# Optimization experiments

Measured on AMD Instinct MI355X. Metric: run time of the kernel, lower is better.

## Reference

```python
import jax, jax.numpy as jnp
import numpy as np

B, S, N, D, O = 64, 512, 128, 768, 3


def _xavier(k, shape):
    lim = (6.0 / (shape[0] + shape[1])) ** 0.5
    return jax.random.uniform(k, shape, jnp.float32, -lim, lim)


def setup_inputs() -> dict:
    key = jax.random.key(0)
    ks = jax.random.split(key, 16)
    sentence_embed = jax.random.normal(ks[0], (B, S, D), jnp.float32)
    # sparse binary dependency-graph adjacencies
    dg = (jax.random.uniform(ks[1], (B, N, N)) < 0.08).astype(jnp.float32)
    dg1 = (jax.random.uniform(ks[2], (B, N, N)) < 0.08).astype(jnp.float32)
    # target token span inside the sentence: [start, end), end > start
    start = jax.random.randint(ks[3], (B,), 1, 400)
    length = jax.random.randint(ks[4], (B,), 1, 16)
    target_span = jnp.stack([start, start + length], -1).astype(jnp.int32)
    # contiguous subword spans per GCN node (tran_indices), non-overlapping
    lens = jax.random.randint(ks[5], (B, N), 1, 4)
    ends = jnp.minimum(jnp.cumsum(lens, axis=1), S - 2)
    starts = jnp.concatenate([jnp.zeros((B, 1), ends.dtype), ends[:, :-1]], axis=1)
    tran_spans = jnp.stack([starts, ends], -1).astype(jnp.int32)  # [B,N,2]
    # node span of the target in the GCN graph (span_indices[i][0])
    gs = jax.random.randint(ks[6], (B,), 0, N - 8)
    gl = jax.random.randint(ks[7], (B,), 1, 8)
    gcn_span = jnp.stack([gs, gs + gl], -1).astype(jnp.int32)
    # parameters
    W_proj = _xavier(ks[8], (D, D))
    Wg1 = _xavier(ks[9], (D, D))
    Wg2 = _xavier(ks[10], (D, D))
    Wg3 = _xavier(ks[11], (D, D))
    stdv = 1.0 / np.sqrt(D)
    bg1 = jax.random.uniform(ks[12], (D,), jnp.float32, -stdv, stdv)
    bg2 = jax.random.uniform(ks[13], (D,), jnp.float32, -stdv, stdv)
    bg3 = jax.random.uniform(ks[14], (D,), jnp.float32, -stdv, stdv)
    fc_W = _xavier(ks[15], (2 * D, O))
    fc_b = jnp.zeros((O,), jnp.float32)
    return dict(sentence_embed=sentence_embed, dg=dg, dg1=dg1, W_proj=W_proj,
                Wg1=Wg1, bg1=bg1, Wg2=Wg2, bg2=bg2, Wg3=Wg3, bg3=bg3,
                fc_W=fc_W, fc_b=fc_b, target_span=target_span,
                tran_spans=tran_spans, gcn_span=gcn_span)


def reference(sentence_embed, dg, dg1, W_proj, Wg1, bg1, Wg2, bg2, Wg3, bg3,
              fc_W, fc_b, target_span, tran_spans, gcn_span):
    dt = sentence_embed.dtype
    pos = jnp.arange(S)
    # --- ragged target max-pool over sentence_embed[l:r] -> [B, D] ---
    tmask = (pos[None, :] >= target_span[:, 0:1]) & (pos[None, :] < target_span[:, 1:2])
    neg = jnp.finfo(dt).min
    target_max = jnp.max(jnp.where(tmask[:, :, None], sentence_embed, neg), axis=1)
    # --- ragged span-sum into GCN node features (tran_indices loop) -> [B, N, D] ---
    # torch slices [s+1 : e+1]
    nmask = ((pos[None, None, :] >= tran_spans[..., 0:1] + 1) &
             (pos[None, None, :] < tran_spans[..., 1:2] + 1)).astype(dt)  # [B,N,S]
    tmps = jnp.einsum('bns,bsd->bnd', nmask, sentence_embed)
    # --- GCN stack (GraphConvolution, bigcn=False) ---
    x = jax.nn.relu(tmps @ W_proj)
    adj = dg + dg1
    adj = jnp.where(adj >= 1, jnp.ones((), dt), adj)
    denom = jnp.sum(adj, axis=2, keepdims=True) + 1e-07
    def gcn(h, W, b):
        return jnp.einsum('bnm,bmd->bnd', adj, h @ W) / denom + b
    x = jax.nn.relu(gcn(x, Wg1, bg1)) + x
    x = jax.nn.relu(gcn(x, Wg2, bg2)) + x
    x = jax.nn.relu(gcn(x, Wg3, bg3)) + x
    # --- ragged node-span sum over GCN output -> [B, D] ---
    npos = jnp.arange(N)
    gmask = ((npos[None, :] >= gcn_span[:, 0:1]) & (npos[None, :] < gcn_span[:, 1:2])).astype(dt)
    gcn_target = jnp.einsum('bn,bnd->bd', gmask, x)
    # --- head ---
    logits = jnp.tanh(jnp.concatenate([target_max, gcn_target], axis=1) @ fc_W + fc_b)
    return logits
```

## Files before the change

kernel.cpp:

```cpp
#include <hip/hip_runtime.h>
#include <float.h>
#include <math.h>

typedef __attribute__((ext_vector_type(8))) short short8;
typedef __attribute__((ext_vector_type(4))) float f32x4;
typedef __attribute__((ext_vector_type(4))) unsigned short u16x4;
typedef unsigned short u16;
typedef unsigned int u32;

constexpr int B_ = 64, S_ = 512, N_ = 128, D_ = 768;

__device__ inline u16 f2h(float x) {
    _Float16 hh = (_Float16)x;
    return __builtin_bit_cast(u16, hh);
}
__device__ inline float h2f(u16 h) {
    return (float)__builtin_bit_cast(_Float16, h);
}

__device__ inline void gload_lds16(const u16* g, u16* s) {
    __builtin_amdgcn_global_load_lds(
        (const __attribute__((address_space(1))) u32*)g,
        (__attribute__((address_space(3))) u32*)s, 16, 0, 0);
}

__device__ inline int fragIdx(int row, int col) {
    return ((row >> 4) * 24 + (col >> 5)) * 512 + ((col >> 3) & 3) * 128
         + (row & 15) * 8 + (col & 7);
}

__global__ __launch_bounds__(192)
void span_split_kernel(const float* __restrict__ se, const int* __restrict__ spans,
                       u16* __restrict__ th) {
    const int bn = blockIdx.x;
    const int b  = bn >> 7;
    const int s  = spans[bn * 2 + 0];
    const int e  = spans[bn * 2 + 1];
    const float* base = se + (size_t)b * S_ * D_;
    const int d4 = threadIdx.x;
    float4 acc = make_float4(0.f, 0.f, 0.f, 0.f);
    for (int r = s + 1; r <= e; ++r) {
        const float4 v = reinterpret_cast<const float4*>(base + (size_t)r * D_)[d4];
        acc.x += v.x; acc.y += v.y; acc.z += v.z; acc.w += v.w;
    }
    u16x4 hv;
    hv[0] = f2h(acc.x); hv[1] = f2h(acc.y);
    hv[2] = f2h(acc.z); hv[3] = f2h(acc.w);
    *(u16x4*)(th + fragIdx(bn, d4 * 4)) = hv;
}

__global__ __launch_bounds__(192)
void target_max_kernel(const float* __restrict__ se, const int* __restrict__ tspan,
                       float* __restrict__ tmax) {
    const int b = blockIdx.x;
    const int c = blockIdx.y * 192 + threadIdx.x;
    const int s = tspan[b * 2 + 0];
    const int e = tspan[b * 2 + 1];
    const float* base = se + (size_t)b * S_ * D_ + c;
    float m = -FLT_MAX;
    for (int r = s; r < e; ++r) m = fmaxf(m, base[(size_t)r * D_]);
    tmax[(size_t)b * D_ + c] = m;
}

__global__ __launch_bounds__(128)
void adj_kernel(const float* __restrict__ dg, const float* __restrict__ dg1,
                u16* __restrict__ adj, float* __restrict__ invden) {
    const int row = blockIdx.x;
    const int t   = threadIdx.x;
    const size_t idx = (size_t)row * N_ + t;
    float a = dg[idx] + dg1[idx];
    a = (a >= 1.f) ? 1.f : a;
    adj[idx] = f2h(a);
    float w = a;
    #pragma unroll
    for (int off = 32; off; off >>= 1) w += __shfl_down(w, off, 64);
    __shared__ float ssum[2];
    if ((t & 63) == 0) ssum[t >> 6] = w;
    __syncthreads();
    if (t == 0) invden[row] = 1.f / (ssum[0] + ssum[1] + 1e-7f);
}

__global__ __launch_bounds__(256)
void wsplit_kernel(const float* __restrict__ W0, const float* __restrict__ W1,
                   const float* __restrict__ W2, const float* __restrict__ W3,
                   u16* __restrict__ wth) {
    __shared__ float t[64][65];
    const int mi = blockIdx.z;
    const float* W = (mi == 0) ? W0 : (mi == 1) ? W1 : (mi == 2) ? W2 : W3;
    const int k0 = blockIdx.y * 64, n0 = blockIdx.x * 64;
    #pragma unroll 4
    for (int it = 0; it < 16; ++it) {
        const int lin = it * 256 + threadIdx.x;
        const int r = lin >> 6, c = lin & 63;
        t[r][c] = W[(size_t)(k0 + r) * D_ + n0 + c];
    }
    __syncthreads();
    u16* oh = wth + (size_t)mi * D_ * D_;
    #pragma unroll 4
    for (int it = 0; it < 16; ++it) {
        const int lin = it * 256 + threadIdx.x;
        const int r = lin >> 6, c = lin & 63;
        oh[(size_t)(n0 + r) * D_ + k0 + c] = f2h(t[c][r]);
    }
}

template<int MODE>
__global__ __launch_bounds__(512, 4)
void gemm_fused(const u16* __restrict__ Ah,
                const u16* __restrict__ Bh,
                const u16* __restrict__ ADJ, const float* __restrict__ invden,
                const float* __restrict__ bias,
                u16* __restrict__ Oh) {
    __shared__ u16 lds[21504];
    const int tid  = threadIdx.x;
    const int lane = tid & 63, w = tid >> 6;
    const int wr = w >> 1, wc = w & 1;
    const int lr = lane & 15, lh = lane >> 4;

    int bid = blockIdx.x;
    bid = (bid & 7) * 64 + (bid >> 3);
    const int bnb = bid & 7, bmb = bid >> 3;
    const int bn = bnb * 96;

    const int qch = (lane & 3) ^ ((lane >> 3) & 3);
    const u16* gBsrc = Bh + (size_t)(bn + w * 16 + (lane >> 2)) * 768 + qch * 8;

    const int mblk0 = bmb * 8 + wr * 2;
    const u16* gAstage = Ah + (size_t)(bmb * 8 + w) * 12288 + lane * 8;

    f32x4 acc[2][3];
    #pragma unroll
    for (int i = 0; i < 2; ++i)
        #pragma unroll
        for (int j = 0; j < 3; ++j)
            acc[i][j] = (f32x4){0.f, 0.f, 0.f, 0.f};

    gload_lds16(gAstage, lds + w * 512);
    if (w < 6) gload_lds16(gBsrc, lds + 12288 + w * 512);
    gload_lds16(gAstage + 512, lds + 4096 + w * 512);
    if (w < 6) gload_lds16(gBsrc + 32, lds + 12288 + 3072 + w * 512);

    const int pB = (lh ^ ((lr >> 1) & 3)) << 3;
    const int aOff0 = (wr * 2) * 512 + lane * 8;
    const int aOff1 = (wr * 2 + 1) * 512 + lane * 8;

#define GEMM_ITER(C)                                                          \
    {                                                                         \
        const int t_ = 3 * tt + (C);                                          \
        if (t_ <= 22) {                                                       \
            if (w < 6) asm volatile("s_waitcnt vmcnt(2)" ::: "memory");       \
            else       asm volatile("s_waitcnt vmcnt(1)" ::: "memory");       \
        } else {                                                              \
            asm volatile("s_waitcnt vmcnt(0)" ::: "memory");                  \
        }                                                                     \
        __builtin_amdgcn_s_barrier();                                         \
        __builtin_amdgcn_sched_barrier(0);                                    \
        if (t_ <= 21) {                                                       \
            gload_lds16(gAstage + (t_ + 2) * 512,                             \
                        lds + (((C) + 2) % 3) * 4096 + w * 512);              \
            if (w < 6)                                                        \
                gload_lds16(gBsrc + (t_ + 2) * 32,                            \
                            lds + 12288 + (((C) + 2) % 3) * 3072 + w * 512);  \
        }                                                                     \
        const u16* La = lds + ((C) % 3) * 4096;                               \
        const u16* Lb = lds + 12288 + ((C) % 3) * 3072;                       \
        short8 aF[2], bF[3];                                                  \
        aF[0] = *(const short8*)&La[aOff0];                                   \
        aF[1] = *(const short8*)&La[aOff1];                                   \
        _Pragma("unroll")                                                     \
        for (int f = 0; f < 3; ++f)                                           \
            bF[f] = *(const short8*)&Lb[(wc * 48 + f * 16 + lr) * 32 + pB];   \
        __builtin_amdgcn_s_setprio(1);                                        \
        _Pragma("unroll")                                                     \
        for (int mf = 0; mf < 2; ++mf)                                        \
            _Pragma("unroll")                                                 \
            for (int nf = 0; nf < 3; ++nf)                                    \
                acc[mf][nf] = __builtin_amdgcn_mfma_f32_16x16x32_f16(aF[mf], bF[nf], acc[mf][nf], 0, 0, 0); \
        __builtin_amdgcn_s_setprio(0);                                        \
    }

    for (int tt = 0; tt < 8; ++tt) {
        GEMM_ITER(0)
        GEMM_ITER(1)
        GEMM_ITER(2)
    }
#undef GEMM_ITER

    if (MODE == 0) {
        #pragma unroll
        for (int mf = 0; mf < 2; ++mf) {
            const int mblk = mblk0 + mf;
            #pragma unroll
            for (int r = 0; r < 4; ++r) {
                const int lane_r = lh * 4 + r;
                #pragma unroll
                for (int nf = 0; nf < 3; ++nf) {
                    const int c = bn + wc * 48 + nf * 16 + lr;
                    const int idx = (mblk * 24 + (c >> 5)) * 512
                                  + ((c >> 3) & 3) * 128 + lane_r * 8 + (c & 7);
                    Oh[idx] = f2h(fmaxf(acc[mf][nf][r], 0.f));
                }
            }
        }
        return;
    }

    __builtin_amdgcn_s_barrier();
    __builtin_amdgcn_sched_barrier(0);

    const u16* adjb = ADJ + (size_t)bmb * (N_ * N_);
    short8 adjr[8];
    #pragma unroll
    for (int mf = 0; mf < 2; ++mf)
        #pragma unroll
        for (int ks = 0; ks < 4; ++ks)
            adjr[mf * 4 + ks] = *(const short8*)(adjb +
                (size_t)(wr * 32 + mf * 16 + lr) * 128 + ks * 32 + lh * 8);

    u16* hwT = lds;
    #pragma unroll
    for (int mf = 0; mf < 2; ++mf) {
        const int node0 = wr * 32 + mf * 16 + lh * 4;
        #pragma unroll
        for (int nf = 0; nf < 3; ++nf) {
            const int c = wc * 48 + nf * 16 + lr;
            u16x4 hv;
            #pragma unroll
            for (int r = 0; r < 4; ++r) hv[r] = f2h(acc[mf][nf][r]);
            *(u16x4*)&hwT[c * 128 + (((node0 >> 3) ^ (c & 7)) << 3) + (node0 & 7)] = hv;
        }
    }
    asm volatile("s_waitcnt lgkmcnt(0)" ::: "memory");
    __builtin_amdgcn_s_barrier();
    __builtin_amdgcn_sched_barrier(0);

    f32x4 acc2[2][3];
    #pragma unroll
    for (int i = 0; i < 2; ++i)
        #pragma unroll
        for (int j = 0; j < 3; ++j)
            acc2[i][j] = (f32x4){0.f, 0.f, 0.f, 0.f};

    #pragma unroll
    for (int ks = 0; ks < 4; ++ks) {
        short8 bf[3];
        #pragma unroll
        for (int f = 0; f < 3; ++f) {
            const int c = wc * 48 + f * 16 + lr;
            bf[f] = *(const short8*)&hwT[c * 128 + (((ks * 4 + lh) ^ (c & 7)) << 3)];
        }
        #pragma unroll
        for (int mf = 0; mf < 2; ++mf)
            #pragma unroll
            for (int nf = 0; nf < 3; ++nf)
                acc2[mf][nf] = __builtin_amdgcn_mfma_f32_16x16x32_f16(adjr[mf * 4 + ks], bf[nf], acc2[mf][nf], 0, 0, 0);
    }

    #pragma unroll
    for (int mf = 0; mf < 2; ++mf) {
        const int mblk = mblk0 + mf;
        #pragma unroll
        for (int r = 0; r < 4; ++r) {
            const int node = wr * 32 + mf * 16 + lh * 4 + r;
            const int lane_r = lh * 4 + r;
            const float inv = invden[bmb * N_ + node];
            #pragma unroll
            for (int nf = 0; nf < 3; ++nf) {
                const int c = bn + wc * 48 + nf * 16 + lr;
                const int idx = (mblk * 24 + (c >> 5)) * 512
                              + ((c >> 3) & 3) * 128 + lane_r * 8 + (c & 7);
                float v = fmaxf(acc2[mf][nf][r] * inv + bias[c], 0.f);
                v += h2f(Ah[idx]);
                Oh[idx] = f2h(v);
            }
        }
    }
}

__global__ __launch_bounds__(192)
void gcn_target_kernel(const u16* __restrict__ Xh,
                       const int* __restrict__ gspan, float* __restrict__ gt) {
    const int b = blockIdx.x;
    const int c = blockIdx.y * 192 + threadIdx.x;
    const int s = gspan[b * 2 + 0];
    const int e = gspan[b * 2 + 1];
    float acc = 0.f;
    for (int n = s; n < e; ++n)
        acc += h2f(Xh[fragIdx(b * N_ + n, c)]);
    gt[(size_t)b * D_ + c] = acc;
}

__global__ __launch_bounds__(256)
void head_kernel(const float* __restrict__ tmax, const float* __restrict__ gt,
                 const float* __restrict__ fcW, const float* __restrict__ fcb,
                 float* __restrict__ out) {
    const int b = blockIdx.x;
    const int t = threadIdx.x;
    float p0 = 0.f, p1 = 0.f, p2 = 0.f;
    for (int i = t; i < 2 * D_; i += 256) {
        const float v = (i < D_) ? tmax[(size_t)b * D_ + i] : gt[(size_t)b * D_ + i - D_];
        p0 += v * fcW[i * 3 + 0];
        p1 += v * fcW[i * 3 + 1];
        p2 += v * fcW[i * 3 + 2];
    }
    #pragma unroll
    for (int off = 32; off; off >>= 1) {
        p0 += __shfl_down(p0, off, 64);
        p1 += __shfl_down(p1, off, 64);
        p2 += __shfl_down(p2, off, 64);
    }
    __shared__ float red[4][3];
    const int wv = t >> 6;
    if ((t & 63) == 0) { red[wv][0] = p0; red[wv][1] = p1; red[wv][2] = p2; }
    __syncthreads();
    if (t == 0) {
        #pragma unroll
        for (int o = 0; o < 3; ++o) {
            const float s = red[0][o] + red[1][o] + red[2][o] + red[3][o] + fcb[o];
            out[b * 3 + o] = tanhf(s);
        }
    }
}

extern "C" void kernel_launch(void* const* d_in, const int* in_sizes, int n_in,
                              void* d_out, int out_size, void* d_ws, size_t ws_size,
                              hipStream_t stream) {
    const float* se   = (const float*)d_in[0];
    const float* dg   = (const float*)d_in[1];
    const float* dg1  = (const float*)d_in[2];
    const float* Wp   = (const float*)d_in[3];
    const float* Wg[3] = {(const float*)d_in[4], (const float*)d_in[6], (const float*)d_in[8]};
    const float* bg[3] = {(const float*)d_in[5], (const float*)d_in[7], (const float*)d_in[9]};
    const float* fcW  = (const float*)d_in[10];
    const float* fcb  = (const float*)d_in[11];
    const int*   tspan  = (const int*)d_in[12];
    const int*   nspans = (const int*)d_in[13];
    const int*   gspan  = (const int*)d_in[14];
    float* out = (float*)d_out;

    u16* us   = (u16*)d_ws;
    u16* X0   = us;
    u16* X1   = X0 + 6291456;
    u16* TH   = X1 + 6291456;
    u16* WTh  = TH + 6291456;
    u16* ADJ  = WTh + 2359296;
    float* INV = (float*)(ADJ + 1048576);
    float* TMX = INV + 8192;
    float* GT  = TMX + 49152;

    span_split_kernel<<<B_ * N_, 192, 0, stream>>>(se, nspans, TH);
    target_max_kernel<<<dim3(B_, 4), 192, 0, stream>>>(se, tspan, TMX);
    adj_kernel<<<B_ * N_, 128, 0, stream>>>(dg, dg1, ADJ, INV);
    wsplit_kernel<<<dim3(12, 12, 4), 256, 0, stream>>>(Wp, Wg[0], Wg[1], Wg[2], WTh);

    gemm_fused<0><<<512, 512, 0, stream>>>(TH, WTh,
                                           nullptr, nullptr, nullptr, X0);

    const u16* in_[3] = {X0, X1, X0};
    u16* out_[3] = {X1, X0, X1};
    for (int l = 0; l < 3; ++l) {
        const size_t wo = (size_t)(l + 1) * D_ * D_;
        gemm_fused<1><<<512, 512, 0, stream>>>(in_[l], WTh + wo,
                                               ADJ, INV, bg[l], out_[l]);
    }

    gcn_target_kernel<<<dim3(B_, 4), 192, 0, stream>>>(X1, gspan, GT);
    head_kernel<<<B_, 256, 0, stream>>>(TMX, GT, fcW, fcb, out);
}
```

Measured before the change: 110.4 us.

## Switch GEMM main loop to double-buffered K=64 steps

The GEMM pipeline changes from a triple-buffered K=32 stage scheme to a double-buffered scheme that loads K=64 per stage, halving the number of barriers and waits per K sweep. Each iteration now waits for all outstanding loads (vmcnt(0)) before the barrier, so prefetch depth drops to a single stage ahead. LDS grows from 21504 to 28672 halfwords per block, which may reduce occupancy under the 4-block launch bound, and fully draining loads each step can expose memory latency.

```diff
diff --git a/kernel.cpp b/kernel.cpp
--- a/kernel.cpp
+++ b/kernel.cpp
@@ -111,7 +111,7 @@
                 const u16* __restrict__ ADJ, const float* __restrict__ invden,
                 const float* __restrict__ bias,
                 u16* __restrict__ Oh) {
-    __shared__ u16 lds[21504];
+    __shared__ u16 lds[28672];
     const int tid  = threadIdx.x;
     const int lane = tid & 63, w = tid >> 6;
     const int wr = w >> 1, wc = w & 1;
@@ -135,54 +135,56 @@
         for (int j = 0; j < 3; ++j)
             acc[i][j] = (f32x4){0.f, 0.f, 0.f, 0.f};
 
-    gload_lds16(gAstage, lds + w * 512);
-    if (w < 6) gload_lds16(gBsrc, lds + 12288 + w * 512);
-    gload_lds16(gAstage + 512, lds + 4096 + w * 512);
-    if (w < 6) gload_lds16(gBsrc + 32, lds + 12288 + 3072 + w * 512);
+    gload_lds16(gAstage,       lds + w * 1024);
+    gload_lds16(gAstage + 512, lds + w * 1024 + 512);
+    if (w < 6) {
+        gload_lds16(gBsrc,      lds + 16384 + w * 512);
+        gload_lds16(gBsrc + 32, lds + 16384 + 3072 + w * 512);
+    }
 
     const int pB = (lh ^ ((lr >> 1) & 3)) << 3;
-    const int aOff0 = (wr * 2) * 512 + lane * 8;
-    const int aOff1 = (wr * 2 + 1) * 512 + lane * 8;
 
 #define GEMM_ITER(C)                                                          \
     {                                                                         \
-        const int t_ = 3 * tt + (C);                                          \
-        if (t_ <= 22) {                                                       \
-            if (w < 6) asm volatile("s_waitcnt vmcnt(2)" ::: "memory");       \
-            else       asm volatile("s_waitcnt vmcnt(1)" ::: "memory");       \
-        } else {                                                              \
-            asm volatile("s_waitcnt vmcnt(0)" ::: "memory");                  \
-        }                                                                     \
+        const int t_ = 2 * tt + (C);                                          \
+        asm volatile("s_waitcnt vmcnt(0)" ::: "memory");                      \
         __builtin_amdgcn_s_barrier();                                         \
         __builtin_amdgcn_sched_barrier(0);                                    \
-        if (t_ <= 21) {                                                       \
-            gload_lds16(gAstage + (t_ + 2) * 512,                             \
-                        lds + (((C) + 2) % 3) * 4096 + w * 512);              \
-            if (w < 6)                                                        \
-                gload_lds16(gBsrc + (t_ + 2) * 32,                            \
-                            lds + 12288 + (((C) + 2) % 3) * 3072 + w * 512);  \
+        if (t_ <= 10) {                                                       \
+            u16* ab = lds + (((C) + 1) & 1) * 8192;                           \
+            gload_lds16(gAstage + (2 * (t_ + 1)) * 512,     ab + w * 1024);   \
+            gload_lds16(gAstage + (2 * (t_ + 1) + 1) * 512, ab + w * 1024 + 512); \
+            if (w < 6) {                                                      \
+                u16* bb = lds + 16384 + (((C) + 1) & 1) * 6144;               \
+                gload_lds16(gBsrc + (t_ + 1) * 64,      bb + w * 512);        \
+                gload_lds16(gBsrc + (t_ + 1) * 64 + 32, bb + 3072 + w * 512); \
+            }                                                                 \
         }                                                                     \
-        const u16* La = lds + ((C) % 3) * 4096;                               \
-        const u16* Lb = lds + 12288 + ((C) % 3) * 3072;                       \
-        short8 aF[2], bF[3];                                                  \
-        aF[0] = *(const short8*)&La[aOff0];                                   \
-        aF[1] = *(const short8*)&La[aOff1];                                   \
+        const u16* La = lds + ((C) & 1) * 8192;                               \
+        const u16* Lb = lds + 16384 + ((C) & 1) * 6144;                       \
+        short8 aF[2][2], bF[3][2];                                            \
         _Pragma("unroll")                                                     \
-        for (int f = 0; f < 3; ++f)                                           \
-            bF[f] = *(const short8*)&Lb[(wc * 48 + f * 16 + lr) * 32 + pB];   \
+        for (int sl = 0; sl < 2; ++sl) {                                      \
+            aF[0][sl] = *(const short8*)&La[(wr * 2) * 1024 + sl * 512 + lane * 8];     \
+            aF[1][sl] = *(const short8*)&La[(wr * 2 + 1) * 1024 + sl * 512 + lane * 8]; \
+            _Pragma("unroll")                                                 \
+            for (int f = 0; f < 3; ++f)                                       \
+                bF[f][sl] = *(const short8*)&Lb[sl * 3072 + (wc * 48 + f * 16 + lr) * 32 + pB]; \
+        }                                                                     \
         __builtin_amdgcn_s_setprio(1);                                        \
         _Pragma("unroll")                                                     \
-        for (int mf = 0; mf < 2; ++mf)                                        \
+        for (int sl = 0; sl < 2; ++sl)                                        \
             _Pragma("unroll")                                                 \
-            for (int nf = 0; nf < 3; ++nf)                                    \
-                acc[mf][nf] = __builtin_amdgcn_mfma_f32_16x16x32_f16(aF[mf], bF[nf], acc[mf][nf], 0, 0, 0); \
+            for (int mf = 0; mf < 2; ++mf)                                    \
+                _Pragma("unroll")                                             \
+                for (int nf = 0; nf < 3; ++nf)                                \
+                    acc[mf][nf] = __builtin_amdgcn_mfma_f32_16x16x32_f16(aF[mf][sl], bF[nf][sl], acc[mf][nf], 0, 0, 0); \
         __builtin_amdgcn_s_setprio(0);                                        \
     }
 
-    for (int tt = 0; tt < 8; ++tt) {
+    for (int tt = 0; tt < 6; ++tt) {
         GEMM_ITER(0)
         GEMM_ITER(1)
-        GEMM_ITER(2)
     }
 #undef GEMM_ITER
 
```

New measurement: 108.7 us. No clear change (-1.6%).
